# Optimization experiments

Hardware: AMD Instinct MI355X
Metric: run time of the kernel (lower is better)

Reference implementation:

```python
import jax, jax.numpy as jnp
import numpy as np

N_NODES = 100000
N_EDGES = 800000
IN_FEAT = 64
HID_FEAT = 64
NUM_CLASS = 16


def _gcn_layer(H, src, dst, W, b, n_nodes):
    # Undirected aggregation: sum neighbor features in both edge directions,
    # plus self-loop, then linear transform.
    agg = (H
           + jax.ops.segment_sum(H[src], dst, num_segments=n_nodes)
           + jax.ops.segment_sum(H[dst], src, num_segments=n_nodes))
    return agg @ W + b


def setup_inputs() -> dict:
    key = jax.random.key(0)
    ks = jax.random.split(key, 8)
    X = jax.random.normal(ks[0], (N_NODES, IN_FEAT), dtype=jnp.float32)
    edge_list = jax.random.randint(ks[1], (2, N_EDGES), 0, N_NODES, dtype=jnp.int32)
    scale = 0.05
    W0 = jax.random.normal(ks[2], (IN_FEAT, HID_FEAT), dtype=jnp.float32) * scale
    W1 = jax.random.normal(ks[3], (HID_FEAT, HID_FEAT), dtype=jnp.float32) * scale
    W2 = jax.random.normal(ks[4], (HID_FEAT, HID_FEAT), dtype=jnp.float32) * scale
    W3 = jax.random.normal(ks[5], (HID_FEAT, NUM_CLASS), dtype=jnp.float32) * scale
    b0 = jnp.zeros((HID_FEAT,), jnp.float32)
    b1 = jnp.zeros((HID_FEAT,), jnp.float32)
    b2 = jnp.zeros((HID_FEAT,), jnp.float32)
    b3 = jnp.zeros((NUM_CLASS,), jnp.float32)
    return {"X": X, "edge_list": edge_list,
            "W0": W0, "b0": b0, "W1": W1, "b1": b1,
            "W2": W2, "b2": b2, "W3": W3, "b3": b3}


def reference(X, edge_list, W0, b0, W1, b1, W2, b2, W3, b3):
    n_nodes = X.shape[0]
    src, dst = edge_list[0], edge_list[1]
    # init layer + ReLU
    H = jax.nn.relu(_gcn_layer(X, src, dst, W0, b0, n_nodes))
    # 2 hidden layers + ReLU
    H = jax.nn.relu(_gcn_layer(H, src, dst, W1, b1, n_nodes))
    H = jax.nn.relu(_gcn_layer(H, src, dst, W2, b2, n_nodes))
    # output layer (no activation)
    H_out = _gcn_layer(H, src, dst, W3, b3, n_nodes)
    # global mean pooling over nodes -> [1, num_class]
    return jnp.mean(H_out, axis=0, keepdims=True)
```

## Files before the change

kernel.cpp:

```cpp
#include <hip/hip_runtime.h>

#define N_NODES 100000
#define N_EDGES 800000
#define NB 391
#define NPB 256
#define CAP 5120
#define BIN_CAP 40
#define EDGES_PER_BLK 2048
#define BIN_GRID ((N_EDGES + EDGES_PER_BLK - 1) / EDGES_PER_BLK)

typedef unsigned int uint32;
typedef float f2x __attribute__((ext_vector_type(2)));

#if __has_builtin(__builtin_amdgcn_cvt_pk_f32_fp8) && __has_builtin(__builtin_amdgcn_cvt_pk_fp8_f32)
#define HW_FP8 1
#endif

__device__ __forceinline__ float fp8_dec_sw(uint32 v) {
    uint32 s = (v & 0x80u) << 24;
    uint32 e = (v >> 3) & 0xFu;
    uint32 m = v & 7u;
    if (e == 0) {
        float f = (float)m * 0.001953125f;
        return (v & 0x80u) ? -f : f;
    }
    return __uint_as_float(s | ((e + 120u) << 23) | (m << 20));
}
__device__ __forceinline__ uint32 fp8_enc_sw(float f) {
    uint32 u = __float_as_uint(f);
    uint32 s = (u >> 24) & 0x80u;
    uint32 a = u & 0x7FFFFFFFu;
    if (a < 0x3C000000u) {
        float af = __uint_as_float(a);
        uint32 m = (uint32)(af * 512.0f + 0.5f);
        if (m > 7u) return s | 0x08u;
        return s | m;
    }
    if (a >= 0x43E00000u) return s | 0x7Eu;
    uint32 r = a + 0x000FFFFFu + ((a >> 20) & 1u);
    uint32 e = (r >> 23) - 120u;
    uint32 m = (r >> 20) & 7u;
    if (e > 15u) return s | 0x7Eu;
    return s | (e << 3) | m;
}

__device__ __forceinline__ void dec4(uint32 v, float* o) {
#ifdef HW_FP8
    f2x lo = __builtin_amdgcn_cvt_pk_f32_fp8((int)v, false);
    f2x hi = __builtin_amdgcn_cvt_pk_f32_fp8((int)v, true);
    o[0] = lo.x; o[1] = lo.y; o[2] = hi.x; o[3] = hi.y;
#else
    o[0] = fp8_dec_sw(v); o[1] = fp8_dec_sw(v >> 8);
    o[2] = fp8_dec_sw(v >> 16); o[3] = fp8_dec_sw(v >> 24);
#endif
}
__device__ __forceinline__ uint32 enc4(float a, float b, float c, float d) {
#ifdef HW_FP8
    int v = 0;
    v = __builtin_amdgcn_cvt_pk_fp8_f32(a, b, v, false);
    v = __builtin_amdgcn_cvt_pk_fp8_f32(c, d, v, true);
    return (uint32)v;
#else
    return fp8_enc_sw(a) | (fp8_enc_sw(b) << 8) | (fp8_enc_sw(c) << 16) | (fp8_enc_sw(d) << 24);
#endif
}
__device__ __forceinline__ void acc16(uint4 h, float* a) {
    float t[16];
    dec4(h.x, t + 0); dec4(h.y, t + 4); dec4(h.z, t + 8); dec4(h.w, t + 12);
#pragma unroll
    for (int j = 0; j < 16; ++j) a[j] += t[j];
}

__global__ void f32_to_fp8_k(const float4* __restrict__ in, uint4* __restrict__ out, int n16) {
    int i = blockIdx.x * blockDim.x + threadIdx.x;
    if (i >= n16) return;
    float4 a = in[4 * i + 0];
    float4 b = in[4 * i + 1];
    float4 c = in[4 * i + 2];
    float4 d = in[4 * i + 3];
    uint4 o;
    o.x = enc4(a.x, a.y, a.z, a.w);
    o.y = enc4(b.x, b.y, b.z, b.w);
    o.z = enc4(c.x, c.y, c.z, c.w);
    o.w = enc4(d.x, d.y, d.z, d.w);
    out[i] = o;
}

__global__ void zero_misc(int* __restrict__ bcnt, float* __restrict__ csum) {
    int i = blockIdx.x * blockDim.x + threadIdx.x;
    if (i < NB) bcnt[i] = 0;
    if (i < 64) csum[i] = 0.f;
}

__global__ void bin_kernel(const int* __restrict__ src, const int* __restrict__ dst,
                           int* __restrict__ bcnt, uint32* __restrict__ bpairs) {
    __shared__ int lcnt[NB];
    __shared__ uint32 lbin[NB * BIN_CAP];
    for (int b = threadIdx.x; b < NB; b += 256) lcnt[b] = 0;
    __syncthreads();

    int base = blockIdx.x * EDGES_PER_BLK;
#pragma unroll
    for (int j = 0; j < EDGES_PER_BLK / 256; ++j) {
        int e = base + j * 256 + threadIdx.x;
        if (e < N_EDGES) {
            int s = src[e], d = dst[e];
            {
                int b = d >> 8;
                uint32 val = ((uint32)(d & 255) << 17) | (uint32)s;
                int pos = atomicAdd(&lcnt[b], 1);
                if (pos < BIN_CAP) lbin[b * BIN_CAP + pos] = val;
                else {
                    int g = atomicAdd(&bcnt[b], 1);
                    if (g < CAP) bpairs[(size_t)b * CAP + g] = val;
                }
            }
            {
                int b = s >> 8;
                uint32 val = ((uint32)(s & 255) << 17) | (uint32)d;
                int pos = atomicAdd(&lcnt[b], 1);
                if (pos < BIN_CAP) lbin[b * BIN_CAP + pos] = val;
                else {
                    int g = atomicAdd(&bcnt[b], 1);
                    if (g < CAP) bpairs[(size_t)b * CAP + g] = val;
                }
            }
        }
    }
    __syncthreads();

    for (int b = threadIdx.x; b < NB; b += 256) {
        int k = lcnt[b];
        if (k > BIN_CAP) k = BIN_CAP;
        int g = 0;
        if (k > 0) g = atomicAdd(&bcnt[b], k);
        lcnt[b] = (g << 6) | k;
    }
    __syncthreads();
    const int TOT = NB * BIN_CAP;
    for (int idx = threadIdx.x; idx < TOT; idx += 256) {
        int b = idx / BIN_CAP;
        int j = idx - b * BIN_CAP;
        int pkv = lcnt[b];
        int k = pkv & 63;
        if (j < k) {
            int gg = (pkv >> 6) + j;
            if (gg < CAP) bpairs[(size_t)b * CAP + gg] = lbin[b * BIN_CAP + j];
        }
    }
}

__global__ void __launch_bounds__(256)
bucket_build(const int* __restrict__ bcnt, const uint32* __restrict__ bpairs,
             int* __restrict__ deg, int* __restrict__ rowptr, int* __restrict__ adj) {
    __shared__ int h[NPB];
    __shared__ int part[NPB];
    __shared__ int stage[CAP];
    __shared__ int sbase;
    int b = blockIdx.x, t = threadIdx.x;

    {
        int x = 0;
        if (t < b) { int v = bcnt[t]; x = (v > CAP) ? CAP : v; }
        int t2 = t + 256;
        if (t2 < b) { int v = bcnt[t2]; x += (v > CAP) ? CAP : v; }
        part[t] = x;
        __syncthreads();
        for (int off = 128; off > 0; off >>= 1) {
            if (t < off) part[t] += part[t + off];
            __syncthreads();
        }
        if (t == 0) sbase = part[0];
        __syncthreads();
    }
    int base = sbase;
    int cnt = bcnt[b];
    if (cnt > CAP) cnt = CAP;

    h[t] = 0;
    __syncthreads();
    for (int i = t; i < cnt; i += 256)
        atomicAdd(&h[bpairs[(size_t)b * CAP + i] >> 17], 1);
    __syncthreads();
    int node = (b << 8) + t;
    int myh = h[t];
    if (node < N_NODES) deg[node] = myh;

    part[t] = myh;
    __syncthreads();
    for (int off = 1; off < 256; off <<= 1) {
        int u = (t >= off) ? part[t - off] : 0;
        __syncthreads();
        part[t] += u;
        __syncthreads();
    }
    int excl = part[t] - myh;
    if (node < N_NODES) rowptr[node] = base + excl;
    if (node == N_NODES - 1) rowptr[N_NODES] = 2 * N_EDGES;

    h[t] = excl;
    __syncthreads();
    for (int i = t; i < cnt; i += 256) {
        uint32 p = bpairs[(size_t)b * CAP + i];
        int ln = (int)(p >> 17);
        int nbr = (int)(p & 0x1FFFFu);
        int slot = atomicAdd(&h[ln], 1);
        if (slot < CAP) stage[slot] = nbr;
    }
    __syncthreads();
    for (int i = t; i < cnt; i += 256) adj[base + i] = stage[i];
}

#define FMA4(ACC, WV) ACC.x += a * (WV).x; ACC.y += a * (WV).y; \
                      ACC.z += a * (WV).z; ACC.w += a * (WV).w;
__global__ void __launch_bounds__(256)
fused_layer(const uint4* __restrict__ Hin,
            const int* __restrict__ rowptr,
            const int* __restrict__ adj,
            const float* __restrict__ W,
            const float* __restrict__ bias,
            uint4* __restrict__ Hout) {
    __shared__ uint4 aggL[64 * 5];

    int node_base = blockIdx.x * 64;
    {
        int n = node_base + (threadIdx.x >> 2);
        int c = threadIdx.x & 3;
        int ln = threadIdx.x >> 2;
        if (n < N_NODES) {
            int beg = rowptr[n], end = rowptr[n + 1];
            float a[16];
            uint4 s = Hin[(size_t)n * 4 + c];
            dec4(s.x, a + 0); dec4(s.y, a + 4); dec4(s.z, a + 8); dec4(s.w, a + 12);
            int i = beg;
            for (; i + 2 <= end; i += 2) {
                int v0 = adj[i];
                int v1 = adj[i + 1];
                uint4 h0 = Hin[(size_t)v0 * 4 + c];
                uint4 h1 = Hin[(size_t)v1 * 4 + c];
                acc16(h0, a);
                acc16(h1, a);
            }
            if (i < end) {
                uint4 h = Hin[(size_t)adj[i] * 4 + c];
                acc16(h, a);
            }
            uint4 o;
            o.x = enc4(a[0], a[1], a[2], a[3]);
            o.y = enc4(a[4], a[5], a[6], a[7]);
            o.z = enc4(a[8], a[9], a[10], a[11]);
            o.w = enc4(a[12], a[13], a[14], a[15]);
            aggL[ln * 5 + c] = o;
        }
    }
    __syncthreads();

    int ln2 = threadIdx.x & 63;
    int c2 = __builtin_amdgcn_readfirstlane(threadIdx.x >> 6);
    int n2 = node_base + ln2;
    if (n2 >= N_NODES) return;

    float4 acc0, acc1, acc2, acc3;
    {
        const float4* b4 = (const float4*)bias + c2 * 4;
        acc0 = b4[0]; acc1 = b4[1]; acc2 = b4[2]; acc3 = b4[3];
    }
    const float4* Wc = (const float4*)(W + c2 * 16);
#pragma unroll
    for (int q = 0; q < 4; ++q) {
        uint4 v = aggL[ln2 * 5 + q];
        float af[16];
        dec4(v.x, af + 0); dec4(v.y, af + 4); dec4(v.z, af + 8); dec4(v.w, af + 12);
#pragma unroll
        for (int k = 0; k < 16; ++k) {
            const float4* wr = Wc + (q * 16 + k) * 16;
            float a = af[k];
            float4 w0 = wr[0], w1 = wr[1], w2 = wr[2], w3 = wr[3];
            FMA4(acc0, w0)
            FMA4(acc1, w1)
            FMA4(acc2, w2)
            FMA4(acc3, w3)
        }
    }

    uint4 o;
    o.x = enc4(fmaxf(acc0.x, 0.f), fmaxf(acc0.y, 0.f), fmaxf(acc0.z, 0.f), fmaxf(acc0.w, 0.f));
    o.y = enc4(fmaxf(acc1.x, 0.f), fmaxf(acc1.y, 0.f), fmaxf(acc1.z, 0.f), fmaxf(acc1.w, 0.f));
    o.z = enc4(fmaxf(acc2.x, 0.f), fmaxf(acc2.y, 0.f), fmaxf(acc2.z, 0.f), fmaxf(acc2.w, 0.f));
    o.w = enc4(fmaxf(acc3.x, 0.f), fmaxf(acc3.y, 0.f), fmaxf(acc3.z, 0.f), fmaxf(acc3.w, 0.f));
    Hout[(size_t)n2 * 4 + c2] = o;
}

__global__ void wcolsum_fp8(const uint32* __restrict__ H32, const int* __restrict__ deg,
                            float* __restrict__ csum) {
    __shared__ float red[256];
    int f = threadIdx.x & 63;
    int r = threadIdx.x >> 6;
    int word = f >> 2;
    int sh = (f & 3) * 8;
    float local = 0.f;
    for (int n = blockIdx.x * 4 + r; n < N_NODES; n += gridDim.x * 4) {
        uint32 v = H32[(size_t)n * 16 + word];
        float h = fp8_dec_sw((v >> sh) & 0xFFu);
        local += (1.0f + (float)deg[n]) * h;
    }
    red[threadIdx.x] = local;
    __syncthreads();
    if (threadIdx.x < 64) {
        float s = red[threadIdx.x] + red[threadIdx.x + 64] +
                  red[threadIdx.x + 128] + red[threadIdx.x + 192];
        atomicAdd(&csum[f], s);
    }
}

__global__ void finalize_kernel(const float* __restrict__ csum,
                                const float* __restrict__ W3,
                                const float* __restrict__ b3,
                                float* __restrict__ out) {
    int j = threadIdx.x;
    if (j >= 16) return;
    const float inv = 1.0f / (float)N_NODES;
    float s = b3[j];
#pragma unroll
    for (int f = 0; f < 64; ++f) s += (csum[f] * inv) * W3[f * 16 + j];
    out[j] = s;
}

extern "C" void kernel_launch(void* const* d_in, const int* in_sizes, int n_in,
                              void* d_out, int out_size, void* d_ws, size_t ws_size,
                              hipStream_t stream) {
    const float* X  = (const float*)d_in[0];
    const int*   el = (const int*)d_in[1];
    const int*   src = el;
    const int*   dst = el + N_EDGES;
    const float* W0 = (const float*)d_in[2];
    const float* b0 = (const float*)d_in[3];
    const float* W1 = (const float*)d_in[4];
    const float* b1 = (const float*)d_in[5];
    const float* W2 = (const float*)d_in[6];
    const float* b2 = (const float*)d_in[7];
    const float* W3 = (const float*)d_in[8];
    const float* b3 = (const float*)d_in[9];
    float* out = (float*)d_out;

    uint32* Xb  = (uint32*)d_ws;
    uint32* B0  = Xb + (size_t)N_NODES * 16;
    uint32* B1  = B0 + (size_t)N_NODES * 16;
    float* csum = (float*)(B1 + (size_t)N_NODES * 16);
    int*   deg      = (int*)(csum + 64);
    int*   rowptr   = deg + N_NODES;
    int*   bcnt     = rowptr + N_NODES + 1;
    uint32* bpairs  = (uint32*)(bcnt + NB);
    int*   adj      = (int*)(bpairs + (size_t)NB * CAP);

    const dim3 blk(256);
    const int convGrid  = (N_NODES * 4 + 255) / 256;
    const int layerGrid = (N_NODES * 4 + 255) / 256;

    f32_to_fp8_k<<<convGrid, blk, 0, stream>>>((const float4*)X, (uint4*)Xb, N_NODES * 4);

    zero_misc<<<(NB + 255) / 256, blk, 0, stream>>>(bcnt, csum);
    bin_kernel<<<BIN_GRID, blk, 0, stream>>>(src, dst, bcnt, bpairs);
    bucket_build<<<NB, blk, 0, stream>>>(bcnt, bpairs, deg, rowptr, adj);

    fused_layer<<<layerGrid, blk, 0, stream>>>((const uint4*)Xb, rowptr, adj, W0, b0, (uint4*)B0);
    fused_layer<<<layerGrid, blk, 0, stream>>>((const uint4*)B0, rowptr, adj, W1, b1, (uint4*)B1);
    fused_layer<<<layerGrid, blk, 0, stream>>>((const uint4*)B1, rowptr, adj, W2, b2, (uint4*)B0);

    wcolsum_fp8<<<1024, blk, 0, stream>>>(B0, deg, csum);
    finalize_kernel<<<1, 64, 0, stream>>>(csum, W3, b3, out);
}
```

Baseline: 198.0 us.

## Stage block adjacency in LDS, unroll gather by four, fold zeroing into conversion

Each layer block now copies its contiguous CSR adjacency segment (up to a fixed cap) into shared memory, so the gather loop reads neighbor indices from LDS instead of global memory. The gather loop is unrolled from two to four neighbors to keep more loads in flight. The separate zeroing kernel is merged into the fp8 conversion kernel, saving one launch. In exchange, each block spends extra LDS and a barrier before aggregation, and a runtime branch selects LDS or global reads.

```diff
diff --git a/kernel.cpp b/kernel.cpp
--- a/kernel.cpp
+++ b/kernel.cpp
@@ -8,6 +8,7 @@
 #define BIN_CAP 40
 #define EDGES_PER_BLK 2048
 #define BIN_GRID ((N_EDGES + EDGES_PER_BLK - 1) / EDGES_PER_BLK)
+#define ADJ_CAP 2048
 
 typedef unsigned int uint32;
 typedef float f2x __attribute__((ext_vector_type(2)));
@@ -71,8 +72,11 @@
     for (int j = 0; j < 16; ++j) a[j] += t[j];
 }
 
-__global__ void f32_to_fp8_k(const float4* __restrict__ in, uint4* __restrict__ out, int n16) {
+__global__ void f32_to_fp8_k(const float4* __restrict__ in, uint4* __restrict__ out, int n16,
+                             int* __restrict__ bcnt, float* __restrict__ csum) {
     int i = blockIdx.x * blockDim.x + threadIdx.x;
+    if (i < NB) bcnt[i] = 0;
+    if (i < 64) csum[i] = 0.f;
     if (i >= n16) return;
     float4 a = in[4 * i + 0];
     float4 b = in[4 * i + 1];
@@ -84,12 +88,6 @@
     o.z = enc4(c.x, c.y, c.z, c.w);
     o.w = enc4(d.x, d.y, d.z, d.w);
     out[i] = o;
-}
-
-__global__ void zero_misc(int* __restrict__ bcnt, float* __restrict__ csum) {
-    int i = blockIdx.x * blockDim.x + threadIdx.x;
-    if (i < NB) bcnt[i] = 0;
-    if (i < 64) csum[i] = 0.f;
 }
 
 __global__ void bin_kernel(const int* __restrict__ src, const int* __restrict__ dst,
@@ -221,8 +219,21 @@
             const float* __restrict__ bias,
             uint4* __restrict__ Hout) {
     __shared__ uint4 aggL[64 * 5];
+    __shared__ int adjL[ADJ_CAP];
 
     int node_base = blockIdx.x * 64;
+    int top = node_base + 64;
+    if (top > N_NODES) top = N_NODES;
+    int seg_beg = rowptr[node_base];
+    int seg_end = rowptr[top];
+    int seg_len = seg_end - seg_beg;
+    bool useL = (seg_len <= ADJ_CAP);
+    if (useL) {
+        for (int i = threadIdx.x; i < seg_len; i += 256)
+            adjL[i] = adj[seg_beg + i];
+    }
+    __syncthreads();
+
     {
         int n = node_base + (threadIdx.x >> 2);
         int c = threadIdx.x & 3;
@@ -232,19 +243,27 @@
             float a[16];
             uint4 s = Hin[(size_t)n * 4 + c];
             dec4(s.x, a + 0); dec4(s.y, a + 4); dec4(s.z, a + 8); dec4(s.w, a + 12);
+#define ADJAT(I) (useL ? adjL[(I) - seg_beg] : adj[(I)])
             int i = beg;
-            for (; i + 2 <= end; i += 2) {
-                int v0 = adj[i];
-                int v1 = adj[i + 1];
+            for (; i + 4 <= end; i += 4) {
+                int v0 = ADJAT(i);
+                int v1 = ADJAT(i + 1);
+                int v2 = ADJAT(i + 2);
+                int v3 = ADJAT(i + 3);
                 uint4 h0 = Hin[(size_t)v0 * 4 + c];
                 uint4 h1 = Hin[(size_t)v1 * 4 + c];
+                uint4 h2 = Hin[(size_t)v2 * 4 + c];
+                uint4 h3 = Hin[(size_t)v3 * 4 + c];
                 acc16(h0, a);
                 acc16(h1, a);
+                acc16(h2, a);
+                acc16(h3, a);
             }
-            if (i < end) {
-                uint4 h = Hin[(size_t)adj[i] * 4 + c];
+            for (; i < end; ++i) {
+                uint4 h = Hin[(size_t)ADJAT(i) * 4 + c];
                 acc16(h, a);
             }
+#undef ADJAT
             uint4 o;
             o.x = enc4(a[0], a[1], a[2], a[3]);
             o.y = enc4(a[4], a[5], a[6], a[7]);
@@ -357,9 +376,9 @@
     const int convGrid  = (N_NODES * 4 + 255) / 256;
     const int layerGrid = (N_NODES * 4 + 255) / 256;
 
-    f32_to_fp8_k<<<convGrid, blk, 0, stream>>>((const float4*)X, (uint4*)Xb, N_NODES * 4);
-
-    zero_misc<<<(NB + 255) / 256, blk, 0, stream>>>(bcnt, csum);
+    f32_to_fp8_k<<<convGrid, blk, 0, stream>>>((const float4*)X, (uint4*)Xb, N_NODES * 4,
+                                               bcnt, csum);
+
     bin_kernel<<<BIN_GRID, blk, 0, stream>>>(src, dst, bcnt, bpairs);
     bucket_build<<<NB, blk, 0, stream>>>(bcnt, bpairs, deg, rowptr, adj);
 
```

New measurement: 194.0 us. 2.0% less time.
